# Kernel optimization log

Measured on AMD Instinct MI355X. Metric: run time of the kernel, lower is better.

Reference implementation:

```python
import jax, jax.numpy as jnp
import numpy as np

B = 16384        # batch size
D = 128          # embedding dim == ln_bot[-1]
N_EMB = 26       # number of sparse tables
VOCAB = 50000    # rows per table
LN_BOT = [13, 512, 256, 128]
LN_TOP = [479, 1024, 1024, 512, 1]
# triangular indices matching: li=[i for i in range(ni) for j in range(i)] (offset=0, no self-interaction)
LI, LJ = np.tril_indices(N_EMB + 1, -1)


def _init_linear(key, n_in, n_out):
    kw, kb = jax.random.split(key)
    lim = 1.0 / np.sqrt(n_in)
    W = jax.random.uniform(kw, (n_in, n_out), minval=-lim, maxval=lim, dtype=jnp.float32)
    b = jax.random.uniform(kb, (n_out,), minval=-lim, maxval=lim, dtype=jnp.float32)
    return W, b


def setup_inputs() -> dict:
    key = jax.random.key(0)
    ks = jax.random.split(key, 3 + len(LN_BOT) - 1 + len(LN_TOP) - 1)
    inp = {
        "dense_x": jax.random.normal(ks[0], (B, LN_BOT[0]), dtype=jnp.float32),
        "indices": jax.random.randint(ks[1], (N_EMB, B), 0, VOCAB),
        "emb_tables": jax.random.normal(ks[2], (N_EMB, VOCAB, D), dtype=jnp.float32) * 0.01,
    }
    k = 3
    for i in range(len(LN_BOT) - 1):
        W, b = _init_linear(ks[k], LN_BOT[i], LN_BOT[i + 1]); k += 1
        inp[f"bot_W{i}"], inp[f"bot_b{i}"] = W, b
    for i in range(len(LN_TOP) - 1):
        W, b = _init_linear(ks[k], LN_TOP[i], LN_TOP[i + 1]); k += 1
        inp[f"top_W{i}"], inp[f"top_b{i}"] = W, b
    return inp


def reference(dense_x, indices, emb_tables,
              bot_W0, bot_b0, bot_W1, bot_b1, bot_W2, bot_b2,
              top_W0, top_b0, top_W1, top_b1, top_W2, top_b2, top_W3, top_b3):
    # bottom MLP (sigmoid_bot=-1 -> all ReLU)
    x = dense_x
    for W, b in ((bot_W0, bot_b0), (bot_W1, bot_b1), (bot_W2, bot_b2)):
        x = jax.nn.relu(x @ W + b)                      # [B, 128]

    # embedding lookups (bag size 1 per table)
    emb = jax.vmap(lambda t, i: t[i])(emb_tables, indices)   # [26, B, D]
    emb = jnp.transpose(emb, (1, 0, 2))                      # [B, 26, D]

    # dot interaction
    T = jnp.concatenate([x[:, None, :], emb], axis=1)        # [B, 27, D]
    Z = jnp.einsum('bid,bjd->bij', T, T)                     # [B, 27, 27]
    Zflat = Z[:, LI, LJ]                                     # [B, 351]
    R = jnp.concatenate([x, Zflat], axis=1)                  # [B, 479]

    # top MLP (sigmoid on last layer, sigmoid_top=3)
    h = R
    for W, b in ((top_W0, top_b0), (top_W1, top_b1), (top_W2, top_b2)):
        h = jax.nn.relu(h @ W + b)
    p = jax.nn.sigmoid(h @ top_W3 + top_b3)                  # [B, 1]
    return jnp.clip(p, 0.0, 1.0)                             # loss_threshold = 0.0
```

## Files before the change

kernel.cpp:

```cpp
#include <hip/hip_runtime.h>

typedef __attribute__((ext_vector_type(8))) short short8;
typedef __attribute__((ext_vector_type(4))) float f32x4;
typedef __attribute__((ext_vector_type(16))) float f32x16;

#define B_ROWS 16384

__device__ __forceinline__ float bf2f(ushort u){ return __uint_as_float(((uint)u)<<16); }
__device__ __forceinline__ ushort f2bf(float f){
  uint u = __float_as_uint(f);
  u = u + 0x7FFFu + ((u>>16)&1u);
  return (ushort)(u>>16);
}
__device__ __forceinline__ void gload_lds16(const void* g, void* l){
  __builtin_amdgcn_global_load_lds((const __attribute__((address_space(1))) unsigned*)g,
                                   (__attribute__((address_space(3))) unsigned*)l, 16, 0, 0);
}

struct TArgs { const float* in; ushort* out; int K, N, Kp; };
struct PrepArgs {
  const float* x; const float* W0; const float* b0; ushort* act0;
  TArgs t[5];
  float* partial;
};

__global__ __launch_bounds__(256) void prep(PrepArgs a)
{
  const int idx = blockIdx.x;
  const int tid = threadIdx.x;
  __shared__ float tile[32][33];

  if (idx < 32768){
    int i = idx*256 + tid;
    int b = i>>9, n = i&511;
    const float* xr = a.x + (size_t)b*13;
    float s = a.b0[n];
    #pragma unroll
    for (int k=0;k<13;k++) s += xr[k]*a.W0[k*512+n];
    a.act0[i] = f2bf(fmaxf(s,0.f));
    return;
  }
  if (idx >= 34976){
    a.partial[(idx-34976)*256 + tid] = 0.f;
    return;
  }
  int t = idx - 32768, s;
  int kx, ny;
  if (t < 128)            { s=0; kx=t%16; ny=t/16; }
  else if ((t-=128) < 32) { s=1; kx=t%8 ; ny=t/8 ; }
  else if ((t-=32) < 512) { s=2; kx=t%16; ny=t/16; }
  else if ((t-=512)<1024) { s=3; kx=t%32; ny=t/32; }
  else                    { s=4; kx=(t-1024)%32; ny=(t-1024)/32; }
  TArgs ta = a.t[s];
  int k0 = kx*32, n0 = ny*32;
  const int c = tid & 31, r8 = tid >> 5;
  #pragma unroll
  for (int p=0;p<4;p++){
    int k = k0 + r8 + p*8;
    tile[r8+p*8][c] = (k < ta.K) ? ta.in[(size_t)k*ta.N + n0 + c] : 0.f;
  }
  __syncthreads();
  #pragma unroll
  for (int p=0;p<4;p++){
    int n = n0 + r8 + p*8;
    ta.out[(size_t)n*ta.Kp + k0 + c] = f2bf(tile[c][r8+p*8]);
  }
}

template<int TM, bool RELU>
__global__ __launch_bounds__(256) void gemm_bt(const ushort* __restrict__ A,
    const ushort* __restrict__ Bt, const float* __restrict__ bias,
    ushort* __restrict__ C, int M, int N, int K, int ldc)
{
  constexpr int BM = TM*32;
  __shared__ __align__(16) ushort lA[2][BM*64];
  __shared__ __align__(16) ushort lB[2][128*64];
  const int tid = threadIdx.x;
  const int wave = tid>>6, lane = tid&63;
  const int bm = blockIdx.x*BM, bn = blockIdx.y*128;
  const int wrr = (wave>>1)*(BM/2), wcc = (wave&1)*64;
  const int lr = lane&15, lg = lane>>4;
  const int nt = K>>6;
  const int obA = wave*(TM*1024) + lane*16;
  const int obB = wave*4096 + lane*16;

  f32x4 acc[TM][4];
  #pragma unroll
  for (int m=0;m<TM;m++)
    #pragma unroll
    for (int n=0;n<4;n++)
      #pragma unroll
      for (int j=0;j<4;j++) acc[m][n][j] = 0.f;

  auto stage = [&](int buf, int kt){
    #pragma unroll
    for (int c=0;c<TM;c++){
      int o = obA + c*1024;
      int row = o>>7, colb = o&127;
      gload_lds16((const char*)A  + (((size_t)(bm+row)*K + (kt<<6))<<1) + colb, (char*)lA[buf] + o);
    }
    #pragma unroll
    for (int c=0;c<4;c++){
      int o = obB + c*1024;
      int row = o>>7, colb = o&127;
      gload_lds16((const char*)Bt + (((size_t)(bn+row)*K + (kt<<6))<<1) + colb, (char*)lB[buf] + o);
    }
  };

  stage(0, 0);
  int cur = 0;
  for (int t=0; t<nt; ++t){
    int nx = (t+1 < nt) ? t+1 : 0;
    stage(cur^1, nx);
    if constexpr (TM==4) asm volatile("s_waitcnt vmcnt(8)" ::: "memory");
    else                 asm volatile("s_waitcnt vmcnt(6)" ::: "memory");
    __builtin_amdgcn_s_barrier();
    asm volatile("" ::: "memory");
    #pragma unroll
    for (int kk=0;kk<64;kk+=32){
      short8 af[TM], bfr[4];
      const int lk = kk + lg*8;
      #pragma unroll
      for (int m=0;m<TM;m++) af[m]  = *(const short8*)&lA[cur][(wrr+m*16+lr)*64 + lk];
      #pragma unroll
      for (int n=0;n<4;n++) bfr[n] = *(const short8*)&lB[cur][(wcc+n*16+lr)*64 + lk];
      #pragma unroll
      for (int m=0;m<TM;m++)
        #pragma unroll
        for (int n=0;n<4;n++)
          acc[m][n] = __builtin_amdgcn_mfma_f32_16x16x32_bf16(af[m], bfr[n], acc[m][n], 0,0,0);
    }
    asm volatile("" ::: "memory");
    __builtin_amdgcn_s_barrier();
    cur ^= 1;
  }

  #pragma unroll
  for (int n=0;n<4;n++){
    int col = bn + wcc + n*16 + lr;
    float bv = bias[col];
    #pragma unroll
    for (int m=0;m<TM;m++){
      #pragma unroll
      for (int j=0;j<4;j++){
        int row = bm + wrr + m*16 + lg*4 + j;
        float v = acc[m][n][j] + bv;
        if (RELU) v = fmaxf(v,0.f);
        C[(size_t)row*ldc + col] = f2bf(v);
      }
    }
  }
}

template<int BN, bool FUSE>
__global__ __launch_bounds__(512, 2) void gemm256(const ushort* __restrict__ A,
    const ushort* __restrict__ Bt, const float* __restrict__ bias,
    ushort* __restrict__ C, int K, int ldc,
    const float* __restrict__ w3, float* __restrict__ partial)
{
  constexpr int  NF = BN/128;
  constexpr int  LB = BN/128;
  constexpr uint BR = (uint)BN*32u;
  constexpr uint BUFSZ = 16384u + 2u*BR;
  __shared__ __align__(16) ushort lds[2*BUFSZ];

  const int tid = threadIdx.x;
  const int wave = tid>>6, lane = tid&63;
  const uint wm = (uint)(wave>>2), wn = (uint)(wave&3);
  const uint lc = (uint)(lane&31), hi = (uint)(lane>>5);
  const int bm = blockIdx.x*256, bn = blockIdx.y*BN;
  const int nt = K>>6, niter = nt>>1;

  f32x16 acc[4][NF];
  #pragma unroll
  for (int m=0;m<4;m++)
    #pragma unroll
    for (int n=0;n<NF;n++)
      #pragma unroll
      for (int j=0;j<16;j++) acc[m][n][j] = 0.f;

  short8 bfr[2][NF];

#define STAGE(MAT, KH, TILE, SBUF) do{                                          \
    int kt_ = (TILE);                                                           \
    int ktc_ = (kt_ < nt) ? kt_ : 0;       \
    const ushort* gb_ = (MAT) ? Bt : A;                                         \
    const uint ro_ = (MAT) ? (uint)bn : (uint)bm;                               \
    const uint rb_ = (uint)(SBUF)*BUFSZ + ((MAT) ? (16384u + (uint)(KH)*BR)     \
                                                 : ((uint)(KH)*8192u));         \
    const int nl_ = (MAT) ? LB : 2;                                             \
    _Pragma("unroll")                                                           \
    for (int j_=0; j_<nl_; ++j_){                                               \
      uint lin_ = (uint)tid*16u + (uint)j_*8192u;                               \
      uint src_ = lin_ ^ (((lin_>>7)&3u)<<4);                                   \
      uint row_ = src_>>6, colb_ = src_&63u;                                    \
      const char* g_ = (const char*)gb_ +                                       \
        (((size_t)(ro_+row_)*(size_t)K + (size_t)ktc_*64 + (KH)*32)<<1) + colb_;\
      gload_lds16(g_, (char*)lds + (size_t)rb_*2 + lin_);                       \
    }                                                                           \
  }while(0)

#define PHASE(CBUF, KKH, MH, BLOAD, SMAT, SKH, STILE, SBUF, CKPT) do{           \
    const uint ab_ = (uint)(CBUF)*BUFSZ + (uint)(KKH)*8192u;                    \
    short8 af_[2][2];                                                           \
    _Pragma("unroll")                                                           \
    for (int mfl_=0; mfl_<2; ++mfl_){                                           \
      uint r_ = wm*128u + ((uint)(MH)*2u+(uint)mfl_)*32u + lc;                  \
      _Pragma("unroll")                                                         \
      for (int k2_=0; k2_<2; ++k2_){                                            \
        uint l_ = r_*64u + hi*16u + (uint)k2_*32u;                              \
        af_[mfl_][k2_] = *(const short8*)((const char*)lds + (size_t)ab_*2      \
                                   + (l_ ^ (((l_>>7)&3u)<<4)));                 \
      }                                                                         \
    }                                                                           \
    if (BLOAD){                                                                 \
      const uint bb_ = (uint)(CBUF)*BUFSZ + 16384u + (uint)(KKH)*BR;            \
      _Pragma("unroll")                                                         \
      for (int nf_=0; nf_<NF; ++nf_){                                           \
        uint r_ = wn*(uint)(BN/4) + (uint)nf_*32u + lc;                         \
        _Pragma("unroll")                                                       \
        for (int k2_=0; k2_<2; ++k2_){                                          \
          uint l_ = r_*64u + hi*16u + (uint)k2_*32u;                            \
          bfr[k2_][nf_] = *(const short8*)((const char*)lds + (size_t)bb_*2     \
                                     + (l_ ^ (((l_>>7)&3u)<<4)));               \
        }                                                                       \
      }                                                                         \
    }                                                                           \
    STAGE(SMAT, SKH, STILE, SBUF);                                              \
    asm volatile("" ::: "memory");                                              \
    __builtin_amdgcn_s_barrier();                                               \
    asm volatile("" ::: "memory");                                              \
    __builtin_amdgcn_s_setprio(1);                                              \
    _Pragma("unroll")                                                           \
    for (int mfl_=0; mfl_<2; ++mfl_)                                            \
      _Pragma("unroll")                                                         \
      for (int nf_=0; nf_<NF; ++nf_)                                            \
        _Pragma("unroll")                                                       \
        for (int k2_=0; k2_<2; ++k2_)                                           \
          acc[(MH)*2+mfl_][nf_] = __builtin_amdgcn_mfma_f32_32x32x16_bf16(      \
              af_[mfl_][k2_], bfr[k2_][nf_], acc[(MH)*2+mfl_][nf_], 0,0,0);     \
    __builtin_amdgcn_s_setprio(0);                                              \
    if (CKPT){                                                                  \
      if constexpr (LB==2) asm volatile("s_waitcnt vmcnt(8)" ::: "memory");     \
      else                 asm volatile("s_waitcnt vmcnt(6)" ::: "memory");     \
    }                                                                           \
    asm volatile("" ::: "memory");                                              \
    __builtin_amdgcn_s_barrier();                                               \
  }while(0)

  STAGE(0,0,0,0); STAGE(1,0,0,0); STAGE(0,1,0,0); STAGE(1,1,0,0);
  STAGE(0,0,1,1); STAGE(1,0,1,1);
  if constexpr (LB==2) asm volatile("s_waitcnt vmcnt(4)" ::: "memory");
  else                 asm volatile("s_waitcnt vmcnt(3)" ::: "memory");
  asm volatile("" ::: "memory");
  __builtin_amdgcn_s_barrier();

  for (int i=0; i<niter; ++i){
    const int O  = 2*i+1;
    const int E2 = 2*i+2;
    const int O2 = 2*i+3;
    PHASE(0,0,0,true , 0,1,O ,1, false);
    PHASE(0,0,1,false, 1,1,O ,1, true );
    PHASE(0,1,0,true , 0,0,E2,0, false);
    PHASE(0,1,1,false, 1,0,E2,0, true );
    PHASE(1,0,0,true , 0,1,E2,0, false);
    PHASE(1,0,1,false, 1,1,E2,0, true );
    PHASE(1,1,0,true , 0,0,O2,1, false);
    PHASE(1,1,1,false, 1,0,O2,1, true );
  }
#undef PHASE
#undef STAGE

  if constexpr (FUSE){
    int col = bn + (int)wn*(BN/4) + (int)lc;
    float bv = bias[col];
    float wv = w3[col];
    #pragma unroll
    for (int mf=0; mf<4; ++mf){
      #pragma unroll
      for (int reg=0; reg<16; ++reg){
        float v = fmaxf(acc[mf][0][reg] + bv, 0.f) * wv;
        #pragma unroll
        for (int off=1; off<32; off<<=1) v += __shfl_xor(v, off);
        if (lc == 0){
          int row = bm + (int)wm*128 + mf*32 + (reg&3) + 8*(reg>>2) + 4*(int)hi;
          atomicAdd(&partial[row], v);
        }
      }
    }
  } else {
    #pragma unroll
    for (int nf=0; nf<NF; ++nf){
      int col = bn + (int)wn*(BN/4) + nf*32 + (int)lc;
      float bv = bias[col];
      #pragma unroll
      for (int mf=0; mf<4; ++mf){
        #pragma unroll
        for (int reg=0; reg<16; ++reg){
          int row = bm + (int)wm*128 + mf*32 + (reg&3) + 8*(reg>>2) + 4*(int)hi;
          float v = acc[mf][nf][reg] + bv;
          C[(size_t)row*ldc + col] = f2bf(fmaxf(v, 0.f));
        }
      }
    }
  }
}

__global__ __launch_bounds__(256) void interact(const int* __restrict__ idx,
    const float* __restrict__ emb, ushort* __restrict__ R)
{
  __shared__ __align__(16) ushort Tl[4][32][136];
  const int w = threadIdx.x>>6, l = threadIdx.x&63;
  const int b = blockIdx.x*4 + w;
  ushort* Rrow = R + (size_t)b*512;

  uint xv = ((const uint*)Rrow)[l];
  *(uint*)&Tl[w][0][2*l] = xv;

  int myidx = (l<26) ? idx[(size_t)l*B_ROWS + b] : 0;
  const int half = l>>5, lc = l&31;
  #pragma unroll
  for (int i=0;i<13;i++){
    const int row = 2*i + 1 + half;
    int e = __shfl(myidx, row - 1);
    const float4* rp = (const float4*)(emb + ((size_t)(row-1)*50000 + (size_t)e)*128);
    float4 v = rp[lc];
    uint2 pk;
    pk.x = (uint)f2bf(v.x) | ((uint)f2bf(v.y)<<16);
    pk.y = (uint)f2bf(v.z) | ((uint)f2bf(v.w)<<16);
    *(uint2*)&Tl[w][row][4*lc] = pk;
  }
  __syncthreads();

  f32x16 acc;
  #pragma unroll
  for (int i=0;i<16;i++) acc[i] = 0.f;
  #pragma unroll
  for (int kk=0;kk<8;kk++){
    short8 fa = *(const short8*)((const char*)&Tl[w][0][0] + (size_t)(l&31)*272 + kk*32 + (l>>5)*16);
    acc = __builtin_amdgcn_mfma_f32_32x32x16_bf16(fa, fa, acc, 0,0,0);
  }

  const int c = l&31;
  #pragma unroll
  for (int j=0;j<16;j++){
    int r = (j&3) + 8*(j>>2) + 4*(l>>5);
    if (c < r && r <= 26) Rrow[128 + r*(r-1)/2 + c] = f2bf(acc[j]);
  }
  if (l < 33) Rrow[479 + l] = 0;
}

__global__ __launch_bounds__(256) void sigm(const float* __restrict__ partial,
    const float* __restrict__ b3, float* __restrict__ out)
{
  int i = blockIdx.x*256 + threadIdx.x;
  float h = partial[i] + b3[0];
  float p = 1.f/(1.f + expf(-h));
  out[i] = fminf(fmaxf(p, 0.f), 1.f);
}

extern "C" void kernel_launch(void* const* d_in, const int* in_sizes, int n_in,
                              void* d_out, int out_size, void* d_ws, size_t ws_size,
                              hipStream_t stream)
{
  const float* dense_x = (const float*)d_in[0];
  const int*   indices = (const int*)d_in[1];
  const float* emb     = (const float*)d_in[2];
  const float* bW0 = (const float*)d_in[3];  const float* bb0 = (const float*)d_in[4];
  const float* bW1 = (const float*)d_in[5];  const float* bb1 = (const float*)d_in[6];
  const float* bW2 = (const float*)d_in[7];  const float* bb2 = (const float*)d_in[8];
  const float* tW0 = (const float*)d_in[9];  const float* tb0 = (const float*)d_in[10];
  const float* tW1 = (const float*)d_in[11]; const float* tb1 = (const float*)d_in[12];
  const float* tW2 = (const float*)d_in[13]; const float* tb2 = (const float*)d_in[14];
  const float* tW3 = (const float*)d_in[15]; const float* tb3 = (const float*)d_in[16];
  float* out = (float*)d_out;
  const int Bn = B_ROWS;

  char* ws = (char*)d_ws;
  size_t o = 0;
  auto alloc = [&](size_t bytes)->char*{ char* r = ws + o; o += (bytes + 255) & ~(size_t)255; return r; };
  ushort* wtB1 = (ushort*)alloc(256*512*2);
  ushort* wtB2 = (ushort*)alloc(128*256*2);
  ushort* wtT0 = (ushort*)alloc(1024*512*2);
  ushort* wtT1 = (ushort*)alloc((size_t)1024*1024*2);
  ushort* wtT2 = (ushort*)alloc(512*1024*2);
  float*  partial = (float*)alloc(B_ROWS*4);
  ushort* P    = (ushort*)alloc((size_t)Bn*512*2);
  ushort* act1 = (ushort*)alloc((size_t)Bn*256*2);
  ushort* h1   = (ushort*)alloc((size_t)Bn*1024*2);
  ushort* h2   = (ushort*)alloc((size_t)Bn*1024*2);
  (void)ws_size; (void)in_sizes; (void)n_in; (void)out_size;

  PrepArgs pa;
  pa.x = dense_x; pa.W0 = bW0; pa.b0 = bb0; pa.act0 = P;
  pa.t[0] = { bW1, wtB1, 512 , 256 , 512  };
  pa.t[1] = { bW2, wtB2, 256 , 128 , 256  };
  pa.t[2] = { tW0, wtT0, 479 , 1024, 512  };
  pa.t[3] = { tW1, wtT1, 1024, 1024, 1024 };
  pa.t[4] = { tW2, wtT2, 1024, 512 , 1024 };
  pa.partial = partial;
  prep<<<35040,256,0,stream>>>(pa);

  gemm_bt<4,true><<<dim3(128,2),256,0,stream>>>(P,    wtB1, bb1, act1, Bn,256,512, 256);
  gemm_bt<2,true><<<dim3(256,1),256,0,stream>>>(act1, wtB2, bb2, P,    Bn,128,256, 512);

  interact<<<Bn/4,256,0,stream>>>(indices, emb, P);

  gemm256<256,false><<<dim3(64,4),512,0,stream>>>(P,  wtT0, tb0, h1, 512 , 1024, nullptr, nullptr);
  gemm256<256,false><<<dim3(64,4),512,0,stream>>>(h1, wtT1, tb1, h2, 1024, 1024, nullptr, nullptr);
  gemm256<128,true ><<<dim3(64,4),512,0,stream>>>(h2, wtT2, tb2, nullptr, 1024, 0, tW3, partial);
  sigm<<<Bn/256,256,0,stream>>>(partial, tb3, out);
}
```

Before: 197.0 us.

## Fuse bottom MLP last layer into interaction kernel; use gemm_bt for top layer 0

```diff
diff --git a/kernel.cpp b/kernel.cpp
--- a/kernel.cpp
+++ b/kernel.cpp
@@ -3,6 +3,7 @@
 typedef __attribute__((ext_vector_type(8))) short short8;
 typedef __attribute__((ext_vector_type(4))) float f32x4;
 typedef __attribute__((ext_vector_type(16))) float f32x16;
+typedef __attribute__((ext_vector_type(4))) ushort ushort4v;
 
 #define B_ROWS 16384
 
@@ -20,7 +21,7 @@
 struct TArgs { const float* in; ushort* out; int K, N, Kp; };
 struct PrepArgs {
   const float* x; const float* W0; const float* b0; ushort* act0;
-  TArgs t[5];
+  TArgs t[4];
   float* partial;
 };
 
@@ -40,17 +41,15 @@
     a.act0[i] = f2bf(fmaxf(s,0.f));
     return;
   }
-  if (idx >= 34976){
-    a.partial[(idx-34976)*256 + tid] = 0.f;
+  if (idx >= 34944){
+    a.partial[(idx-34944)*256 + tid] = 0.f;
     return;
   }
-  int t = idx - 32768, s;
-  int kx, ny;
-  if (t < 128)            { s=0; kx=t%16; ny=t/16; }
-  else if ((t-=128) < 32) { s=1; kx=t%8 ; ny=t/8 ; }
-  else if ((t-=32) < 512) { s=2; kx=t%16; ny=t/16; }
-  else if ((t-=512)<1024) { s=3; kx=t%32; ny=t/32; }
-  else                    { s=4; kx=(t-1024)%32; ny=(t-1024)/32; }
+  int t = idx - 32768, s, kx, ny;
+  if (t < 128)              { s=0; kx=t&15; ny=t>>4; }
+  else if ((t-=128) < 512)  { s=1; kx=t&15; ny=t>>4; }
+  else if ((t-=512) < 1024) { s=2; kx=t&31; ny=t>>5; }
+  else { t-=1024;             s=3; kx=t&31; ny=t>>5; }
   TArgs ta = a.t[s];
   int k0 = kx*32, n0 = ny*32;
   const int c = tid & 31, r8 = tid >> 5;
@@ -183,7 +182,7 @@
 
 #define STAGE(MAT, KH, TILE, SBUF) do{                                          \
     int kt_ = (TILE);                                                           \
-    int ktc_ = (kt_ < nt) ? kt_ : 0;       \
+    int ktc_ = (kt_ < nt) ? kt_ : 0;                                            \
     const ushort* gb_ = (MAT) ? Bt : A;                                         \
     const uint ro_ = (MAT) ? (uint)bn : (uint)bm;                               \
     const uint rb_ = (uint)(SBUF)*BUFSZ + ((MAT) ? (16384u + (uint)(KH)*BR)     \
@@ -307,15 +306,42 @@
 }
 
 __global__ __launch_bounds__(256) void interact(const int* __restrict__ idx,
-    const float* __restrict__ emb, ushort* __restrict__ R)
+    const float* __restrict__ emb, const ushort* __restrict__ act1,
+    const float* __restrict__ W2, const float* __restrict__ b2,
+    ushort* __restrict__ R)
 {
   __shared__ __align__(16) ushort Tl[4][32][136];
+  __shared__ __align__(16) ushort A1[4][256];
   const int w = threadIdx.x>>6, l = threadIdx.x&63;
   const int b = blockIdx.x*4 + w;
   ushort* Rrow = R + (size_t)b*512;
 
-  uint xv = ((const uint*)Rrow)[l];
-  *(uint*)&Tl[w][0][2*l] = xv;
+  {
+    int r = threadIdx.x>>6, c4 = (threadIdx.x&63)*4;
+    *(ushort4v*)&A1[r][c4] = *(const ushort4v*)(act1 + (size_t)(blockIdx.x*4+r)*256 + c4);
+  }
+  __syncthreads();
+
+  {
+    const int j = w*32 + (l&31);
+    const int rA = l>>5, rB = rA + 2;
+    float sA = b2[j], sB = b2[j];
+    #pragma unroll 4
+    for (int c=0;c<32;c++){
+      short8 aA = *(const short8*)&A1[rA][8*c];
+      short8 aB = *(const short8*)&A1[rB][8*c];
+      #pragma unroll
+      for (int q=0;q<8;q++){
+        float wv = W2[(size_t)(8*c+q)*128 + j];
+        sA += bf2f((ushort)aA[q]) * wv;
+        sB += bf2f((ushort)aB[q]) * wv;
+      }
+    }
+    ushort xA = f2bf(fmaxf(sA,0.f)), xB = f2bf(fmaxf(sB,0.f));
+    Tl[rA][0][j] = xA;  Tl[rB][0][j] = xB;
+    R[(size_t)(blockIdx.x*4+rA)*512 + j] = xA;
+    R[(size_t)(blockIdx.x*4+rB)*512 + j] = xB;
+  }
 
   int myidx = (l<26) ? idx[(size_t)l*B_ROWS + b] : 0;
   const int half = l>>5, lc = l&31;
@@ -380,7 +406,6 @@
   size_t o = 0;
   auto alloc = [&](size_t bytes)->char*{ char* r = ws + o; o += (bytes + 255) & ~(size_t)255; return r; };
   ushort* wtB1 = (ushort*)alloc(256*512*2);
-  ushort* wtB2 = (ushort*)alloc(128*256*2);
   ushort* wtT0 = (ushort*)alloc(1024*512*2);
   ushort* wtT1 = (ushort*)alloc((size_t)1024*1024*2);
   ushort* wtT2 = (ushort*)alloc(512*1024*2);
@@ -394,19 +419,17 @@
   PrepArgs pa;
   pa.x = dense_x; pa.W0 = bW0; pa.b0 = bb0; pa.act0 = P;
   pa.t[0] = { bW1, wtB1, 512 , 256 , 512  };
-  pa.t[1] = { bW2, wtB2, 256 , 128 , 256  };
-  pa.t[2] = { tW0, wtT0, 479 , 1024, 512  };
-  pa.t[3] = { tW1, wtT1, 1024, 1024, 1024 };
-  pa.t[4] = { tW2, wtT2, 1024, 512 , 1024 };
+  pa.t[1] = { tW0, wtT0, 479 , 1024, 512  };
+  pa.t[2] = { tW1, wtT1, 1024, 1024, 1024 };
+  pa.t[3] = { tW2, wtT2, 1024, 512 , 1024 };
   pa.partial = partial;
-  prep<<<35040,256,0,stream>>>(pa);
-
-  gemm_bt<4,true><<<dim3(128,2),256,0,stream>>>(P,    wtB1, bb1, act1, Bn,256,512, 256);
-  gemm_bt<2,true><<<dim3(256,1),256,0,stream>>>(act1, wtB2, bb2, P,    Bn,128,256, 512);
-
-  interact<<<Bn/4,256,0,stream>>>(indices, emb, P);
-
-  gemm256<256,false><<<dim3(64,4),512,0,stream>>>(P,  wtT0, tb0, h1, 512 , 1024, nullptr, nullptr);
+  prep<<<35008,256,0,stream>>>(pa);
+
+  gemm_bt<4,true><<<dim3(128,2),256,0,stream>>>(P, wtB1, bb1, act1, Bn,256,512, 256);
+
+  interact<<<Bn/4,256,0,stream>>>(indices, emb, act1, bW2, bb2, P);
+
+  gemm_bt<4,true><<<dim3(128,8),256,0,stream>>>(P, wtT0, tb0, h1, Bn,1024,512, 1024);
   gemm256<256,false><<<dim3(64,4),512,0,stream>>>(h1, wtT1, tb1, h2, 1024, 1024, nullptr, nullptr);
   gemm256<128,true ><<<dim3(64,4),512,0,stream>>>(h2, wtT2, tb2, nullptr, 1024, 0, tW3, partial);
   sigm<<<Bn/256,256,0,stream>>>(partial, tb3, out);
```

New measurement: 229.0 us. +16.3%, slower.
